# Kernel optimization log

Measured on AMD Instinct MI355X. Metric: run time of the kernel, lower is better.

The kernel has to match this reference:

```python
import jax, jax.numpy as jnp
import numpy as np

B, T, H = 32, 4096, 256

def setup_inputs() -> dict:
    key = jax.random.key(0)
    k1, k2, k3, k4, k5 = jax.random.split(key, 5)
    hidden = jax.random.normal(k1, (B, H), dtype=jnp.float32)
    encoder_outputs = jax.random.normal(k2, (T, B, H), dtype=jnp.float32)
    # nn.Linear(2H, H): weight [H, 2H], bias [H] (kaiming-uniform-ish scale)
    bound = 1.0 / np.sqrt(2 * H)
    attn_w = jax.random.uniform(k3, (H, 2 * H), minval=-bound, maxval=bound, dtype=jnp.float32)
    attn_b = jax.random.uniform(k4, (H,), minval=-bound, maxval=bound, dtype=jnp.float32)
    v = jax.random.uniform(k5, (H,), dtype=jnp.float32)  # torch.rand -> U[0,1)
    return {"hidden": hidden, "encoder_outputs": encoder_outputs,
            "attn_w": attn_w, "attn_b": attn_b, "v": v}

def reference(hidden, encoder_outputs, attn_w, attn_b, v):
    # hidden: [B, H]; encoder_outputs: [T, B, H]
    t = encoder_outputs.shape[0]
    enc = jnp.transpose(encoder_outputs, (1, 0, 2))            # [B, T, H]
    h = jnp.broadcast_to(hidden[:, None, :], enc.shape)        # [B, T, H]
    temp = jnp.concatenate([h, enc], axis=2)                   # [B, T, 2H]
    energy = jax.nn.relu(jnp.einsum('btk,hk->bth', temp, attn_w) + attn_b)  # [B, T, H]
    scores = jnp.einsum('bth,h->bt', energy, v)                # [B, T]
    return jax.nn.softmax(scores, axis=1)[:, None, :]          # [B, 1, T]
```

## Files before the change

### kernel.cpp

```cpp
#include <hip/hip_runtime.h>
#include <hip/hip_bf16.h>

#define B_SZ 32
#define T_SZ 4096
#define H_SZ 256
#define M_SZ (T_SZ * B_SZ)
#define SROW 72

typedef __attribute__((ext_vector_type(8))) short bf16x8;
typedef __attribute__((ext_vector_type(4))) float f32x4;

static __device__ __forceinline__ short f2bf(float x) {
    unsigned u = __float_as_uint(x);
    u += 0x7fffu + ((u >> 16) & 1u);
    return (short)(u >> 16);
}

static __device__ __forceinline__ bf16x8 cvt8(f32x4 a, f32x4 b) {
    bf16x8 r;
    r[0] = f2bf(a[0]); r[1] = f2bf(a[1]); r[2] = f2bf(a[2]); r[3] = f2bf(a[3]);
    r[4] = f2bf(b[0]); r[5] = f2bf(b[1]); r[6] = f2bf(b[2]); r[7] = f2bf(b[3]);
    return r;
}

__global__ __launch_bounds__(256) void prep_kernel(
    const float* __restrict__ hidden, const float* __restrict__ attn_w,
    const float* __restrict__ attn_b, float* __restrict__ hpT,
    short* __restrict__ wbf)
{
    const int h   = blockIdx.x;
    const int tid = threadIdx.x;
    __shared__ float wsh[H_SZ];

    wsh[tid] = attn_w[(size_t)h * 512 + tid];
    wbf[(size_t)h * H_SZ + tid] = f2bf(attn_w[(size_t)h * 512 + 256 + tid]);
    __syncthreads();

    const int b  = tid >> 3;
    const int kg = tid & 7;
    const float* hrow = hidden + b * H_SZ + kg * 32;
    const float* wrow = wsh + kg * 32;
    float s = 0.f;
#pragma unroll
    for (int j = 0; j < 32; j += 4) {
        f32x4 hv = *(const f32x4*)(hrow + j);
        s = fmaf(hv[0], wrow[j + 0], s);
        s = fmaf(hv[1], wrow[j + 1], s);
        s = fmaf(hv[2], wrow[j + 2], s);
        s = fmaf(hv[3], wrow[j + 3], s);
    }
#pragma unroll
    for (int off = 1; off < 8; off <<= 1) s += __shfl_xor(s, off, 8);
    if (kg == 0) hpT[h * B_SZ + b] = s + attn_b[h];
}

__global__ __launch_bounds__(256, 3) void attn_main(
    const float* __restrict__ enc,
    const short* __restrict__ wbf,
    const float* __restrict__ hpT,
    const float* __restrict__ v,
    float* __restrict__ scores)
{
    __shared__ __align__(16) short As[2][64 * SROW];
    __shared__ float part[4][64];

    const int blk  = blockIdx.x;
    const int m0   = blk << 6;
    const int tid  = threadIdx.x;
    const int w    = tid >> 6;
    const int lane = tid & 63;
    const int r    = lane & 15;
    const int quad = lane >> 4;
    const int hbase = w * 64;

    const int srow = tid >> 2, sq = tid & 3;
    const float* sp = enc + (size_t)(m0 + srow) * H_SZ + sq * 16;
    short* sd0 = &As[0][0] + srow * SROW + sq * 16;
    short* sd1 = &As[1][0] + srow * SROW + sq * 16;

    const short* wp0 = wbf + (size_t)(hbase + 0 * 16 + r) * H_SZ + quad * 8;
    const short* wp1 = wbf + (size_t)(hbase + 1 * 16 + r) * H_SZ + quad * 8;
    const short* wp2 = wbf + (size_t)(hbase + 2 * 16 + r) * H_SZ + quad * 8;
    const short* wp3 = wbf + (size_t)(hbase + 3 * 16 + r) * H_SZ + quad * 8;

    f32x4 acc[4][4];
#pragma unroll
    for (int mt = 0; mt < 4; ++mt)
#pragma unroll
        for (int nt = 0; nt < 4; ++nt)
            acc[mt][nt] = (f32x4){0.f, 0.f, 0.f, 0.f};

    bf16x8 bc[2][4];
#pragma unroll
    for (int s = 0; s < 2; ++s) {
        bc[s][0] = *(const bf16x8*)(wp0 + s * 32);
        bc[s][1] = *(const bf16x8*)(wp1 + s * 32);
        bc[s][2] = *(const bf16x8*)(wp2 + s * 32);
        bc[s][3] = *(const bf16x8*)(wp3 + s * 32);
    }
    {
        f32x4 st[4];
#pragma unroll
        for (int j = 0; j < 4; ++j) st[j] = *(const f32x4*)(sp + 4 * j);
        ((bf16x8*)sd0)[0] = cvt8(st[0], st[1]);
        ((bf16x8*)sd0)[1] = cvt8(st[2], st[3]);
    }
    __syncthreads();

#pragma unroll
    for (int kc = 0; kc < 4; ++kc) {
        f32x4 stn[4];
        if (kc < 3) {
#pragma unroll
            for (int j = 0; j < 4; ++j)
                stn[j] = *(const f32x4*)(sp + (kc + 1) * 64 + 4 * j);
        }

        const short* abase = &As[kc & 1][0] + quad * 8;
#pragma unroll
        for (int s = 0; s < 2; ++s) {
            bf16x8 af[4];
#pragma unroll
            for (int mt = 0; mt < 4; ++mt)
                af[mt] = *(const bf16x8*)(abase + (mt * 16 + r) * SROW + s * 32);
#pragma unroll
            for (int mt = 0; mt < 4; ++mt)
#pragma unroll
                for (int nt = 0; nt < 4; ++nt)
                    acc[mt][nt] = __builtin_amdgcn_mfma_f32_16x16x32_bf16(
                        af[mt], bc[s][nt], acc[mt][nt], 0, 0, 0);
        }

        if (kc < 3) {
            const int ko = (kc + 1) * 64;
#pragma unroll
            for (int s = 0; s < 2; ++s) {
                bc[s][0] = *(const bf16x8*)(wp0 + ko + s * 32);
                bc[s][1] = *(const bf16x8*)(wp1 + ko + s * 32);
                bc[s][2] = *(const bf16x8*)(wp2 + ko + s * 32);
                bc[s][3] = *(const bf16x8*)(wp3 + ko + s * 32);
            }
            short* d = ((kc + 1) & 1) ? sd1 : sd0;
            ((bf16x8*)d)[0] = cvt8(stn[0], stn[1]);
            ((bf16x8*)d)[1] = cvt8(stn[2], stn[3]);
            __syncthreads();
        }
    }

    float vv[4];
    f32x4 hpv[2][4];
#pragma unroll
    for (int nt = 0; nt < 4; ++nt) {
        const int h = hbase + nt * 16 + r;
        vv[nt] = v[h];
        hpv[0][nt] = *(const f32x4*)(hpT + h * B_SZ + quad * 4);
        hpv[1][nt] = *(const f32x4*)(hpT + h * B_SZ + 16 + quad * 4);
    }

#pragma unroll
    for (int mt = 0; mt < 4; ++mt) {
#pragma unroll
        for (int reg = 0; reg < 4; ++reg) {
            float s = 0.f;
#pragma unroll
            for (int nt = 0; nt < 4; ++nt) {
                float e = hpv[mt & 1][nt][reg] + acc[mt][nt][reg];
                e = fmaxf(e, 0.f);
                s = fmaf(vv[nt], e, s);
            }
#pragma unroll
            for (int off = 1; off < 16; off <<= 1) s += __shfl_xor(s, off, 16);
            if (r == 0) part[w][mt * 16 + quad * 4 + reg] = s;
        }
    }
    __syncthreads();
    if (tid < 64) {
        float sc = part[0][tid] + part[1][tid] + part[2][tid] + part[3][tid];
        const int b = tid & 31;
        const int t = (m0 + tid) >> 5;
        scores[b * T_SZ + t] = sc;
    }
}

__global__ __launch_bounds__(1024) void softmax_kernel(
    const float* __restrict__ scores, float* __restrict__ out)
{
    const int b   = blockIdx.x;
    const int tid = threadIdx.x;
    const float* s = scores + b * T_SZ;
    float*       o = out    + b * T_SZ;

    float loc[4];
    float m = -3.0e38f;
#pragma unroll
    for (int i = 0; i < 4; ++i) {
        loc[i] = s[tid + i * 1024];
        m = fmaxf(m, loc[i]);
    }
    __shared__ float redm[16], reds[16];
#pragma unroll
    for (int off = 32; off > 0; off >>= 1) m = fmaxf(m, __shfl_xor(m, off, 64));
    if ((tid & 63) == 0) redm[tid >> 6] = m;
    __syncthreads();
#pragma unroll
    for (int i = 0; i < 16; ++i) m = fmaxf(m, redm[i]);

    float sum = 0.f;
#pragma unroll
    for (int i = 0; i < 4; ++i) {
        loc[i] = __expf(loc[i] - m);
        sum += loc[i];
    }
#pragma unroll
    for (int off = 32; off > 0; off >>= 1) sum += __shfl_xor(sum, off, 64);
    if ((tid & 63) == 0) reds[tid >> 6] = sum;
    __syncthreads();
    sum = 0.f;
#pragma unroll
    for (int i = 0; i < 16; ++i) sum += reds[i];
    const float inv = 1.0f / sum;
#pragma unroll
    for (int i = 0; i < 4; ++i) o[tid + i * 1024] = loc[i] * inv;
}

extern "C" void kernel_launch(void* const* d_in, const int* in_sizes, int n_in,
                              void* d_out, int out_size, void* d_ws, size_t ws_size,
                              hipStream_t stream) {
    const float* hidden = (const float*)d_in[0];
    const float* enc    = (const float*)d_in[1];
    const float* attn_w = (const float*)d_in[2];
    const float* attn_b = (const float*)d_in[3];
    const float* v      = (const float*)d_in[4];
    float* out = (float*)d_out;

    float* hpT    = (float*)d_ws;
    float* scores = hpT + H_SZ * B_SZ;
    short* wbf    = (short*)(scores + B_SZ * T_SZ);

    hipLaunchKernelGGL(prep_kernel, dim3(H_SZ), dim3(256), 0, stream,
                       hidden, attn_w, attn_b, hpT, wbf);
    hipLaunchKernelGGL(attn_main, dim3(M_SZ / 64), dim3(256), 0, stream,
                       enc, wbf, hpT, v, scores);
    hipLaunchKernelGGL(softmax_kernel, dim3(B_SZ), dim3(1024), 0, stream,
                       scores, out);
}
```

Before: 226.4 us.

## Pre-swizzle bf16 weights into MFMA fragment order and coalesce encoder loads

The prep kernel now writes the bf16 copy of the encoder half of attn_w in an order that matches the MFMA B-fragment layout, so each lane reads a contiguous 16-byte chunk and a wavefront's weight loads become fully contiguous. The staging of encoder rows into shared memory is reorganised so 16 threads cover a 64-float row segment with float4 loads, and each thread handles four rows spaced 16 apart. This gives contiguous 256-byte global reads per row instead of strided 64-byte pieces. The trade-off is more, smaller 8-byte LDS stores per thread and a more complex index mapping in prep.

Result: faster. 217.8 us (-3.8%).

```diff
diff --git a/kernel.cpp b/kernel.cpp
--- a/kernel.cpp
+++ b/kernel.cpp
@@ -8,6 +8,7 @@
 #define SROW 72
 
 typedef __attribute__((ext_vector_type(8))) short bf16x8;
+typedef __attribute__((ext_vector_type(4))) short bf16x4;
 typedef __attribute__((ext_vector_type(4))) float f32x4;
 
 static __device__ __forceinline__ short f2bf(float x) {
@@ -16,24 +17,29 @@
     return (short)(u >> 16);
 }
 
-static __device__ __forceinline__ bf16x8 cvt8(f32x4 a, f32x4 b) {
-    bf16x8 r;
+static __device__ __forceinline__ bf16x4 cvt4(f32x4 a) {
+    bf16x4 r;
     r[0] = f2bf(a[0]); r[1] = f2bf(a[1]); r[2] = f2bf(a[2]); r[3] = f2bf(a[3]);
-    r[4] = f2bf(b[0]); r[5] = f2bf(b[1]); r[6] = f2bf(b[2]); r[7] = f2bf(b[3]);
     return r;
 }
 
 __global__ __launch_bounds__(256) void prep_kernel(
     const float* __restrict__ hidden, const float* __restrict__ attn_w,
     const float* __restrict__ attn_b, float* __restrict__ hpT,
-    short* __restrict__ wbf)
+    short* __restrict__ wbf2)
 {
     const int h   = blockIdx.x;
     const int tid = threadIdx.x;
     __shared__ float wsh[H_SZ];
 
     wsh[tid] = attn_w[(size_t)h * 512 + tid];
-    wbf[(size_t)h * H_SZ + tid] = f2bf(attn_w[(size_t)h * 512 + 256 + tid]);
+    {
+        const int k = tid;
+        const int hs = h >> 6, nt = (h >> 4) & 3, r = h & 15;
+        const int s = k >> 5, quad = (k >> 3) & 3, e = k & 7;
+        wbf2[(hs * 4 + nt) * 4096 + s * 512 + quad * 128 + r * 8 + e] =
+            f2bf(attn_w[(size_t)h * 512 + 256 + k]);
+    }
     __syncthreads();
 
     const int b  = tid >> 3;
@@ -56,7 +62,7 @@
 
 __global__ __launch_bounds__(256, 3) void attn_main(
     const float* __restrict__ enc,
-    const short* __restrict__ wbf,
+    const short* __restrict__ wbf2,
     const float* __restrict__ hpT,
     const float* __restrict__ v,
     float* __restrict__ scores)
@@ -73,15 +79,14 @@
     const int quad = lane >> 4;
     const int hbase = w * 64;
 
-    const int srow = tid >> 2, sq = tid & 3;
-    const float* sp = enc + (size_t)(m0 + srow) * H_SZ + sq * 16;
-    short* sd0 = &As[0][0] + srow * SROW + sq * 16;
-    short* sd1 = &As[1][0] + srow * SROW + sq * 16;
-
-    const short* wp0 = wbf + (size_t)(hbase + 0 * 16 + r) * H_SZ + quad * 8;
-    const short* wp1 = wbf + (size_t)(hbase + 1 * 16 + r) * H_SZ + quad * 8;
-    const short* wp2 = wbf + (size_t)(hbase + 2 * 16 + r) * H_SZ + quad * 8;
-    const short* wp3 = wbf + (size_t)(hbase + 3 * 16 + r) * H_SZ + quad * 8;
+    const int sr  = tid >> 4;
+    const int sc4 = (tid & 15) * 4;
+    const float* sp = enc + (size_t)(m0 + sr) * H_SZ + sc4;
+    short* sdB[2];
+    sdB[0] = &As[0][0] + sr * SROW + sc4;
+    sdB[1] = &As[1][0] + sr * SROW + sc4;
+
+    const short* wp = wbf2 + (size_t)w * 16384 + lane * 8;
 
     f32x4 acc[4][4];
 #pragma unroll
@@ -90,59 +95,58 @@
         for (int nt = 0; nt < 4; ++nt)
             acc[mt][nt] = (f32x4){0.f, 0.f, 0.f, 0.f};
 
+    f32x4 g[4];
+#pragma unroll
+    for (int i = 0; i < 4; ++i) g[i] = *(const f32x4*)(sp + i * 16 * H_SZ);
+
     bf16x8 bc[2][4];
 #pragma unroll
-    for (int s = 0; s < 2; ++s) {
-        bc[s][0] = *(const bf16x8*)(wp0 + s * 32);
-        bc[s][1] = *(const bf16x8*)(wp1 + s * 32);
-        bc[s][2] = *(const bf16x8*)(wp2 + s * 32);
-        bc[s][3] = *(const bf16x8*)(wp3 + s * 32);
-    }
-    {
-        f32x4 st[4];
-#pragma unroll
-        for (int j = 0; j < 4; ++j) st[j] = *(const f32x4*)(sp + 4 * j);
-        ((bf16x8*)sd0)[0] = cvt8(st[0], st[1]);
-        ((bf16x8*)sd0)[1] = cvt8(st[2], st[3]);
-    }
+    for (int ss = 0; ss < 2; ++ss)
+#pragma unroll
+        for (int nt = 0; nt < 4; ++nt)
+            bc[ss][nt] = *(const bf16x8*)(wp + nt * 4096 + ss * 512);
+
+#pragma unroll
+    for (int i = 0; i < 4; ++i)
+        *(bf16x4*)(sdB[0] + i * 16 * SROW) = cvt4(g[i]);
     __syncthreads();
 
 #pragma unroll
     for (int kc = 0; kc < 4; ++kc) {
-        f32x4 stn[4];
+        f32x4 gn[4];
         if (kc < 3) {
 #pragma unroll
-            for (int j = 0; j < 4; ++j)
-                stn[j] = *(const f32x4*)(sp + (kc + 1) * 64 + 4 * j);
+            for (int i = 0; i < 4; ++i)
+                gn[i] = *(const f32x4*)(sp + i * 16 * H_SZ + (kc + 1) * 64);
         }
 
         const short* abase = &As[kc & 1][0] + quad * 8;
 #pragma unroll
-        for (int s = 0; s < 2; ++s) {
+        for (int ss = 0; ss < 2; ++ss) {
             bf16x8 af[4];
 #pragma unroll
             for (int mt = 0; mt < 4; ++mt)
-                af[mt] = *(const bf16x8*)(abase + (mt * 16 + r) * SROW + s * 32);
+                af[mt] = *(const bf16x8*)(abase + (mt * 16 + r) * SROW + ss * 32);
 #pragma unroll
             for (int mt = 0; mt < 4; ++mt)
 #pragma unroll
                 for (int nt = 0; nt < 4; ++nt)
                     acc[mt][nt] = __builtin_amdgcn_mfma_f32_16x16x32_bf16(
-                        af[mt], bc[s][nt], acc[mt][nt], 0, 0, 0);
+                        af[mt], bc[ss][nt], acc[mt][nt], 0, 0, 0);
         }
 
         if (kc < 3) {
-            const int ko = (kc + 1) * 64;
-#pragma unroll
-            for (int s = 0; s < 2; ++s) {
-                bc[s][0] = *(const bf16x8*)(wp0 + ko + s * 32);
-                bc[s][1] = *(const bf16x8*)(wp1 + ko + s * 32);
-                bc[s][2] = *(const bf16x8*)(wp2 + ko + s * 32);
-                bc[s][3] = *(const bf16x8*)(wp3 + ko + s * 32);
-            }
-            short* d = ((kc + 1) & 1) ? sd1 : sd0;
-            ((bf16x8*)d)[0] = cvt8(stn[0], stn[1]);
-            ((bf16x8*)d)[1] = cvt8(stn[2], stn[3]);
+            const int ko = (kc + 1) * 2;
+#pragma unroll
+            for (int ss = 0; ss < 2; ++ss)
+#pragma unroll
+                for (int nt = 0; nt < 4; ++nt)
+                    bc[ss][nt] = *(const bf16x8*)(wp + nt * 4096 + (ko + ss) * 512);
+
+            short* d = sdB[(kc + 1) & 1];
+#pragma unroll
+            for (int i = 0; i < 4; ++i)
+                *(bf16x4*)(d + i * 16 * SROW) = cvt4(gn[i]);
             __syncthreads();
         }
     }
@@ -235,12 +239,12 @@
 
     float* hpT    = (float*)d_ws;
     float* scores = hpT + H_SZ * B_SZ;
-    short* wbf    = (short*)(scores + B_SZ * T_SZ);
+    short* wbf2   = (short*)(scores + B_SZ * T_SZ);
 
     hipLaunchKernelGGL(prep_kernel, dim3(H_SZ), dim3(256), 0, stream,
-                       hidden, attn_w, attn_b, hpT, wbf);
+                       hidden, attn_w, attn_b, hpT, wbf2);
     hipLaunchKernelGGL(attn_main, dim3(M_SZ / 64), dim3(256), 0, stream,
-                       enc, wbf, hpT, v, scores);
+                       enc, wbf2, hpT, v, scores);
     hipLaunchKernelGGL(softmax_kernel, dim3(B_SZ), dim3(1024), 0, stream,
                        scores, out);
 }
```
